# Kernel optimization log

Measured on AMD Instinct MI355X. Metric: run time of the kernel, lower is better.

Reference implementation:

```python
import jax, jax.numpy as jnp
import numpy as np

DIM = 192
HEADS = 8
B, H, W = 8, 128, 128

def _dwconv3x3(x, w):
    # x: [B,C,H,W], w: [C,1,3,3] depthwise
    return jax.lax.conv_general_dilated(
        x, w, window_strides=(1, 1), padding=((1, 1), (1, 1)),
        dimension_numbers=('NCHW', 'OIHW', 'NCHW'),
        feature_group_count=x.shape[1])

def _proj(x, pw, dw):
    # 1x1 pointwise (as einsum) followed by 3x3 depthwise
    y = jnp.einsum('bchw,oc->bohw', x, pw)
    return _dwconv3x3(y, dw)

def setup_inputs() -> dict:
    key = jax.random.key(0)
    ks = jax.random.split(key, 9)
    s_pw = 1.0 / np.sqrt(DIM)
    s_dw = 1.0 / 3.0
    return {
        'x_feat': jax.random.normal(ks[0], (B, DIM, H, W), jnp.float32),
        'y_feat': jax.random.normal(ks[1], (B, DIM, H, W), jnp.float32),
        'q_pw': jax.random.normal(ks[2], (DIM, DIM), jnp.float32) * s_pw,
        'q_dw': jax.random.normal(ks[3], (DIM, 1, 3, 3), jnp.float32) * s_dw,
        'k_pw': jax.random.normal(ks[4], (DIM, DIM), jnp.float32) * s_pw,
        'k_dw': jax.random.normal(ks[5], (DIM, 1, 3, 3), jnp.float32) * s_dw,
        'v_pw': jax.random.normal(ks[6], (DIM, DIM), jnp.float32) * s_pw,
        'v_dw': jax.random.normal(ks[7], (DIM, 1, 3, 3), jnp.float32) * s_dw,
        'proj_w': jax.random.normal(ks[8], (DIM, DIM), jnp.float32) * s_pw,
        'temperature': jnp.ones((HEADS, 1, 1), jnp.float32),
    }

def reference(x_feat, y_feat, q_pw, q_dw, k_pw, k_dw, v_pw, v_dw, proj_w, temperature):
    b, c, h, w = x_feat.shape
    ch = c // HEADS  # channels per head
    q = _proj(x_feat, q_pw, q_dw)
    k = _proj(y_feat, k_pw, k_dw)
    v = _proj(y_feat, v_pw, v_dw)
    # b (head c) h w -> b head c (h w)
    to_heads = lambda t: t.reshape(b, HEADS, ch, h * w)
    q, k, v = to_heads(q), to_heads(k), to_heads(v)
    # L2-normalize along token dim (torch F.normalize eps=1e-12)
    q = q / jnp.maximum(jnp.linalg.norm(q, axis=-1, keepdims=True), 1e-12)
    k = k / jnp.maximum(jnp.linalg.norm(k, axis=-1, keepdims=True), 1e-12)
    attn = jnp.einsum('bhcn,bhdn->bhcd', q, k) * temperature  # [b,heads,ch,ch]
    attn = jax.nn.softmax(attn, axis=-1)
    out = jnp.einsum('bhcd,bhdn->bhcn', attn, v)
    out = out.reshape(b, c, h, w)
    out = jnp.einsum('bchw,oc->bohw', out, proj_w)
    return out
```

## Files before the change

### kernel.cpp

```cpp
#include <hip/hip_runtime.h>
#include <hip/hip_bf16.h>

#define BATCH 8
#define CDIM 192
#define HEADS 8
#define CH 24
#define HH 128
#define WW 128
#define NPIX (HH*WW)
#define NELEM (BATCH*CDIM*NPIX)
#define NP4 (NPIX/4)

#define DSLAB 16
#define NJOBS 624

typedef __attribute__((ext_vector_type(8))) short bf16x8;
typedef __attribute__((ext_vector_type(4))) float f32x4;
typedef __attribute__((ext_vector_type(4))) unsigned int u32x4;
typedef __attribute__((ext_vector_type(8))) unsigned short u16x8;

#define UNIT 100663296ull
__device__ __align__(256) unsigned char g_pool[4 * UNIT + (16u << 20)];

#define OFF_T0   (0 * UNIT)
#define OFF_QB   (1 * UNIT)
#define OFF_KB   (2 * UNIT)
#define OFF_V    (3 * UNIT)
#define OFF_MISC (4 * UNIT)
#define OFF_PART (OFF_MISC)
#define OFF_S    (OFF_MISC + 2555904ull)
#define OFF_M    (OFF_S + 159744ull)
#define OFF_MF   (OFF_M + 1179648ull)

__device__ inline unsigned short bf_rne(float x) {
  unsigned u = __float_as_uint(x);
  unsigned r = (u + 0x7fffu + ((u >> 16) & 1u)) >> 16;
  return (unsigned short)r;
}
__device__ inline void f32_split(float x, unsigned short& h, unsigned short& l) {
  h = bf_rne(x);
  float hf = __uint_as_float(((unsigned)h) << 16);
  l = bf_rne(x - hf);
}

__global__ __launch_bounds__(64) void w_to_frag(const float* __restrict__ W,
                                                unsigned short* __restrict__ F,
                                                int nb) {
  const int b = blockIdx.x / 12, mf = blockIdx.x % 12;
  const int lane = threadIdx.x;
  const int row = mf * 16 + (lane & 15);
  const size_t lo = (size_t)nb * CDIM * CDIM;
#pragma unroll
  for (int ks = 0; ks < 6; ++ks) {
    const int k0 = ks * 32 + (lane >> 4) * 8;
    const float* src = W + ((size_t)b * CDIM + row) * CDIM + k0;
    bf16x8 hv, lv;
#pragma unroll
    for (int j = 0; j < 8; ++j) {
      unsigned short h, l;
      f32_split(src[j], h, l);
      hv[j] = (short)h;
      lv[j] = (short)l;
    }
    const size_t didx = (((size_t)(blockIdx.x) * 6 + ks) * 64 + lane) * 8;
    *(bf16x8*)(F + didx) = hv;
    *(bf16x8*)(F + lo + didx) = lv;
  }
}

__global__ __launch_bounds__(256, 2) void mfma_gemm192(
    const float* __restrict__ X,
    const unsigned short* __restrict__ WF, size_t w_lo,
    int w_bstride,
    float* __restrict__ Out) {
  const int bn = blockIdx.x;
  const int b = blockIdx.y;
  const int t = threadIdx.x;
  const int lane = t & 63, wid = t >> 6;
  const int wm = wid >> 1, wn = wid & 1;
  const int kq = lane >> 4;

  __shared__ float Xs[32][132];

  const size_t wbase = (size_t)b * w_bstride;
  const float* Xb = X + (size_t)b * CDIM * NPIX;
  const int col4 = (t & 31) * 4;
  const int r0 = t >> 5;
  const int pxl = wn * 64 + (lane & 15);

  f32x4 acc[6][4];
#pragma unroll
  for (int mi = 0; mi < 6; ++mi)
#pragma unroll
    for (int ni = 0; ni < 4; ++ni) acc[mi][ni] = (f32x4){0.f, 0.f, 0.f, 0.f};

  for (int ks = 0; ks < 6; ++ks) {
    float4 st[4];
#pragma unroll
    for (int p = 0; p < 4; ++p)
      st[p] = *(const float4*)(Xb + (size_t)(ks * 32 + r0 + 8 * p) * NPIX +
                               bn * 128 + col4);
#pragma unroll
    for (int p = 0; p < 4; ++p)
      *(float4*)&Xs[r0 + 8 * p][col4 ^ ((p & 1) << 4)] = st[p];
    __syncthreads();

    bf16x8 Ah[6], Al[6];
#pragma unroll
    for (int mi = 0; mi < 6; ++mi) {
      const int mf = wm * 6 + mi;
      const size_t idx = wbase + (((size_t)(mf * 6 + ks)) * 64 + lane) * 8;
      Ah[mi] = *(const bf16x8*)(WF + idx);
      Al[mi] = *(const bf16x8*)(WF + w_lo + idx);
    }

    u32x4 Bh[4], Bl[4];
#pragma unroll
    for (int ni = 0; ni < 4; ++ni) {
      const int pxs = (pxl + ni * 16) ^ ((kq & 1) << 4);
#pragma unroll
      for (int jp = 0; jp < 4; ++jp) {
        const float x0 = Xs[kq * 8 + 2 * jp][pxs];
        const float x1 = Xs[kq * 8 + 2 * jp + 1][pxs];
        const unsigned u0 = __float_as_uint(x0);
        const unsigned u1 = __float_as_uint(x1);
        Bh[ni][jp] = (u1 & 0xffff0000u) | (u0 >> 16);
        const float rr0 = x0 - __uint_as_float(u0 & 0xffff0000u);
        const float rr1 = x1 - __uint_as_float(u1 & 0xffff0000u);
        Bl[ni][jp] = ((unsigned)bf_rne(rr1) << 16) | (unsigned)bf_rne(rr0);
      }
    }
    __syncthreads();

#pragma unroll
    for (int mi = 0; mi < 6; ++mi)
#pragma unroll
      for (int ni = 0; ni < 4; ++ni) {
        const bf16x8 bh = __builtin_bit_cast(bf16x8, Bh[ni]);
        const bf16x8 bl = __builtin_bit_cast(bf16x8, Bl[ni]);
        acc[mi][ni] = __builtin_amdgcn_mfma_f32_16x16x32_bf16(
            Ah[mi], bh, acc[mi][ni], 0, 0, 0);
        acc[mi][ni] = __builtin_amdgcn_mfma_f32_16x16x32_bf16(
            Ah[mi], bl, acc[mi][ni], 0, 0, 0);
        acc[mi][ni] = __builtin_amdgcn_mfma_f32_16x16x32_bf16(
            Al[mi], bh, acc[mi][ni], 0, 0, 0);
      }
  }

  const int ocol = bn * 128 + wn * 64 + (lane & 15);
  const int orow = wm * 96 + (lane >> 4) * 4;
#pragma unroll
  for (int mi = 0; mi < 6; ++mi)
#pragma unroll
    for (int r = 0; r < 4; ++r) {
      const int och = orow + mi * 16 + r;
      float* dst = Out + ((size_t)b * CDIM + och) * NPIX + ocol;
#pragma unroll
      for (int ni = 0; ni < 4; ++ni) dst[ni * 16] = acc[mi][ni][r];
    }
}

__global__ __launch_bounds__(256) void dwconv(const float* __restrict__ In,
                                              const float* __restrict__ Wd,
                                              float* __restrict__ Out) {
  const int idx = blockIdx.x * 256 + threadIdx.x;
  const int x8 = (idx & 15) * 8;
  const int y = (idx >> 4) & 127;
  const int c = (idx >> 11) % CDIM;
  const int b = idx / (2048 * CDIM);

  const float* base = In + (size_t)(b * CDIM + c) * NPIX;
  float w[9];
#pragma unroll
  for (int i = 0; i < 9; ++i) w[i] = Wd[c * 9 + i];

  float a[8] = {0.f, 0.f, 0.f, 0.f, 0.f, 0.f, 0.f, 0.f};
#pragma unroll
  for (int dy = 0; dy < 3; ++dy) {
    const int yy = y + dy - 1;
    if (yy < 0 || yy > 127) continue;
    const float* row = base + yy * WW;
    const float lf = (x8 > 0) ? row[x8 - 1] : 0.f;
    const float4 m0 = *(const float4*)(row + x8);
    const float4 m1 = *(const float4*)(row + x8 + 4);
    const float rt = (x8 + 8 < WW) ? row[x8 + 8] : 0.f;
    const float w0 = w[dy * 3 + 0], w1 = w[dy * 3 + 1], w2 = w[dy * 3 + 2];
    a[0] += w0 * lf   + w1 * m0.x + w2 * m0.y;
    a[1] += w0 * m0.x + w1 * m0.y + w2 * m0.z;
    a[2] += w0 * m0.y + w1 * m0.z + w2 * m0.w;
    a[3] += w0 * m0.z + w1 * m0.w + w2 * m1.x;
    a[4] += w0 * m0.w + w1 * m1.x + w2 * m1.y;
    a[5] += w0 * m1.x + w1 * m1.y + w2 * m1.z;
    a[6] += w0 * m1.y + w1 * m1.z + w2 * m1.w;
    a[7] += w0 * m1.z + w1 * m1.w + w2 * rt;
  }
  float4 o0, o1;
  o0.x = a[0]; o0.y = a[1]; o0.z = a[2]; o0.w = a[3];
  o1.x = a[4]; o1.y = a[5]; o1.z = a[6]; o1.w = a[7];
  *(float4*)(Out + (size_t)idx * 8) = o0;
  *(float4*)(Out + (size_t)idx * 8 + 4) = o1;
}

__global__ __launch_bounds__(256) void dwconv_bf(const float* __restrict__ In,
                                                 const float* __restrict__ Wd,
                                                 unsigned short* __restrict__ Out) {
  const int idx = blockIdx.x * 256 + threadIdx.x;
  const int x8 = (idx & 15) * 8;
  const int y = (idx >> 4) & 127;
  const int c = (idx >> 11) % CDIM;
  const int b = idx / (2048 * CDIM);

  const float* base = In + (size_t)(b * CDIM + c) * NPIX;
  float w[9];
#pragma unroll
  for (int i = 0; i < 9; ++i) w[i] = Wd[c * 9 + i];

  float a[8] = {0.f, 0.f, 0.f, 0.f, 0.f, 0.f, 0.f, 0.f};
#pragma unroll
  for (int dy = 0; dy < 3; ++dy) {
    const int yy = y + dy - 1;
    if (yy < 0 || yy > 127) continue;
    const float* row = base + yy * WW;
    const float lf = (x8 > 0) ? row[x8 - 1] : 0.f;
    const float4 m0 = *(const float4*)(row + x8);
    const float4 m1 = *(const float4*)(row + x8 + 4);
    const float rt = (x8 + 8 < WW) ? row[x8 + 8] : 0.f;
    const float w0 = w[dy * 3 + 0], w1 = w[dy * 3 + 1], w2 = w[dy * 3 + 2];
    a[0] += w0 * lf   + w1 * m0.x + w2 * m0.y;
    a[1] += w0 * m0.x + w1 * m0.y + w2 * m0.z;
    a[2] += w0 * m0.y + w1 * m0.z + w2 * m0.w;
    a[3] += w0 * m0.z + w1 * m0.w + w2 * m1.x;
    a[4] += w0 * m0.w + w1 * m1.x + w2 * m1.y;
    a[5] += w0 * m1.x + w1 * m1.y + w2 * m1.z;
    a[6] += w0 * m1.y + w1 * m1.z + w2 * m1.w;
    a[7] += w0 * m1.z + w1 * m1.w + w2 * rt;
  }
  u16x8 hv, lv;
#pragma unroll
  for (int j = 0; j < 8; ++j) {
    unsigned short h, l;
    f32_split(a[j], h, l);
    hv[j] = h;
    lv[j] = l;
  }
  *(u16x8*)(Out + (size_t)idx * 8) = hv;
  *(u16x8*)(Out + NELEM + (size_t)idx * 8) = lv;
}

__global__ __launch_bounds__(256) void dots_mfma(
    const unsigned short* __restrict__ QF,
    const unsigned short* __restrict__ KF,
    float* __restrict__ Part) {
  const int bh = blockIdx.x;
  const int slab = blockIdx.y;
  const int b = bh >> 3, h = bh & 7;
  const int t = threadIdx.x;
  const int lane = t & 63, wid = t >> 6;

  const size_t rowbase = (size_t)(b * CDIM + h * CH);
  const int px0 = slab * 1024 + wid * 256;
  const int rr = lane & 15;
  const int j8 = (lane >> 4) * 8;

  f32x4 accx[2][2], aqq[2], aqhl[2], akk[2], akhl[2];
#pragma unroll
  for (int mi = 0; mi < 2; ++mi) {
#pragma unroll
    for (int ni = 0; ni < 2; ++ni) accx[mi][ni] = (f32x4){0.f, 0.f, 0.f, 0.f};
    aqq[mi] = (f32x4){0.f, 0.f, 0.f, 0.f};
    aqhl[mi] = (f32x4){0.f, 0.f, 0.f, 0.f};
    akk[mi] = (f32x4){0.f, 0.f, 0.f, 0.f};
    akhl[mi] = (f32x4){0.f, 0.f, 0.f, 0.f};
  }

  auto load_step = [&](int s, bf16x8 (&qh)[2], bf16x8 (&ql)[2],
                       bf16x8 (&kh)[2], bf16x8 (&kl)[2]) {
    const int px = px0 + s * 32 + j8;
#pragma unroll
    for (int mi = 0; mi < 2; ++mi) {
      const size_t off = (rowbase + mi * 16 + rr) * (size_t)NPIX + px;
      qh[mi] = *(const bf16x8*)(QF + off);
      ql[mi] = *(const bf16x8*)(QF + NELEM + off);
      kh[mi] = *(const bf16x8*)(KF + off);
      kl[mi] = *(const bf16x8*)(KF + NELEM + off);
    }
  };
  auto mfma_step = [&](bf16x8 (&qh)[2], bf16x8 (&ql)[2], bf16x8 (&kh)[2],
                       bf16x8 (&kl)[2]) {
#pragma unroll
    for (int mi = 0; mi < 2; ++mi) {
#pragma unroll
      for (int ni = 0; ni < 2; ++ni) {
        accx[mi][ni] = __builtin_amdgcn_mfma_f32_16x16x32_bf16(
            qh[mi], kh[ni], accx[mi][ni], 0, 0, 0);
        accx[mi][ni] = __builtin_amdgcn_mfma_f32_16x16x32_bf16(
            qh[mi], kl[ni], accx[mi][ni], 0, 0, 0);
        accx[mi][ni] = __builtin_amdgcn_mfma_f32_16x16x32_bf16(
            ql[mi], kh[ni], accx[mi][ni], 0, 0, 0);
      }
      aqq[mi] = __builtin_amdgcn_mfma_f32_16x16x32_bf16(qh[mi], qh[mi],
                                                        aqq[mi], 0, 0, 0);
      aqhl[mi] = __builtin_amdgcn_mfma_f32_16x16x32_bf16(qh[mi], ql[mi],
                                                         aqhl[mi], 0, 0, 0);
      akk[mi] = __builtin_amdgcn_mfma_f32_16x16x32_bf16(kh[mi], kh[mi],
                                                        akk[mi], 0, 0, 0);
      akhl[mi] = __builtin_amdgcn_mfma_f32_16x16x32_bf16(kh[mi], kl[mi],
                                                         akhl[mi], 0, 0, 0);
    }
  };

  bf16x8 Aqh[2], Aql[2], Akh[2], Akl[2];
  bf16x8 Bqh[2], Bql[2], Bkh[2], Bkl[2];
  load_step(0, Aqh, Aql, Akh, Akl);
#pragma unroll
  for (int s = 0; s < 8; s += 2) {
    if (s + 1 < 8) load_step(s + 1, Bqh, Bql, Bkh, Bkl);
    mfma_step(Aqh, Aql, Akh, Akl);
    if (s + 2 < 8) load_step(s + 2, Aqh, Aql, Akh, Akl);
    mfma_step(Bqh, Bql, Bkh, Bkl);
  }

  __shared__ float xls[4][24][24];
  __shared__ float qls[4][24], kls[4][24];
  const int col = lane & 15;
  const int rbase = (lane >> 4) * 4;
#pragma unroll
  for (int mi = 0; mi < 2; ++mi) {
#pragma unroll
    for (int ni = 0; ni < 2; ++ni) {
      const int d = ni * 16 + col;
      if (d < 24) {
#pragma unroll
        for (int r = 0; r < 4; ++r) {
          const int c = mi * 16 + rbase + r;
          if (c < 24) xls[wid][c][d] = accx[mi][ni][r];
        }
      }
    }
    const int cc = mi * 16 + col;
    const int rd = col - rbase;
    if (cc < 24 && rd >= 0 && rd < 4) {
      qls[wid][cc] = aqq[mi][rd] + 2.f * aqhl[mi][rd];
      kls[wid][cc] = akk[mi][rd] + 2.f * akhl[mi][rd];
    }
  }
  __syncthreads();

  float* P = Part + ((size_t)bh * DSLAB + slab) * NJOBS;
  for (int j = t; j < 576; j += 256) {
    const int c = j / 24, d = j % 24;
    P[j] = xls[0][c][d] + xls[1][c][d] + xls[2][c][d] + xls[3][c][d];
  }
  if (t < 24) P[576 + t] = qls[0][t] + qls[1][t] + qls[2][t] + qls[3][t];
  else if (t >= 32 && t < 56) {
    const int c = t - 32;
    P[600 + c] = kls[0][c] + kls[1][c] + kls[2][c] + kls[3][c];
  }
}

__global__ __launch_bounds__(640) void dots_reduce(const float* __restrict__ Part,
                                                   float* __restrict__ S) {
  const int bh = blockIdx.x;
  const int job = threadIdx.x;
  if (job >= NJOBS) return;
  float s = 0.f;
  for (int i = 0; i < DSLAB; ++i)
    s += Part[((size_t)bh * DSLAB + i) * NJOBS + job];
  S[bh * NJOBS + job] = s;
}

__global__ __launch_bounds__(576) void build_M(const float* __restrict__ S,
                                               const float* __restrict__ PW,
                                               const float* __restrict__ Temp,
                                               float* __restrict__ M) {
  const int b = blockIdx.x, h = blockIdx.y;
  const int bh = b * 8 + h;
  __shared__ float att[CH][CH];
  __shared__ float qn[CH], kn[CH];
  const int t = threadIdx.x;
  const float* Sb = S + (size_t)bh * NJOBS;

  if (t < CH) {
    qn[t] = fmaxf(sqrtf(Sb[576 + t]), 1e-12f);
    kn[t] = fmaxf(sqrtf(Sb[600 + t]), 1e-12f);
  }
  __syncthreads();
  const float temp = Temp[h];
  if (t < 576) {
    const int c = t / 24, d = t % 24;
    att[c][d] = Sb[t] / (qn[c] * kn[d]) * temp;
  }
  __syncthreads();
  if (t < CH) {
    float mx = -1e30f;
    for (int d = 0; d < CH; ++d) mx = fmaxf(mx, att[t][d]);
    float sum = 0.f;
    for (int d = 0; d < CH; ++d) {
      const float e = __expf(att[t][d] - mx);
      att[t][d] = e;
      sum += e;
    }
    const float inv = 1.f / sum;
    for (int d = 0; d < CH; ++d) att[t][d] *= inv;
  }
  __syncthreads();
  for (int i = t; i < CDIM * CH; i += 576) {
    const int o = i / CH, d = i % CH;
    float s = 0.f;
#pragma unroll
    for (int c = 0; c < CH; ++c) s += PW[o * CDIM + h * CH + c] * att[c][d];
    M[((size_t)b * CDIM + o) * CDIM + h * CH + d] = s;
  }
}


extern "C" void kernel_launch(void* const* d_in, const int* in_sizes, int n_in,
                              void* d_out, int out_size, void* d_ws, size_t ws_size,
                              hipStream_t stream) {
  const float* x_feat = (const float*)d_in[0];
  const float* y_feat = (const float*)d_in[1];
  const float* q_pw   = (const float*)d_in[2];
  const float* q_dw   = (const float*)d_in[3];
  const float* k_pw   = (const float*)d_in[4];
  const float* k_dw   = (const float*)d_in[5];
  const float* v_pw   = (const float*)d_in[6];
  const float* v_dw   = (const float*)d_in[7];
  const float* proj_w = (const float*)d_in[8];
  const float* temp   = (const float*)d_in[9];
  float* out = (float*)d_out;

  unsigned char* pool;
  (void)hipGetSymbolAddress((void**)&pool, HIP_SYMBOL(g_pool));
  float* t0 = (float*)(pool + OFF_T0);
  unsigned short* QB = (unsigned short*)(pool + OFF_QB);
  unsigned short* KB = (unsigned short*)(pool + OFF_KB);
  float* v  = (float*)(pool + OFF_V);
  float* part = (float*)(pool + OFF_PART);
  float* S    = (float*)(pool + OFF_S);
  float* M    = (float*)(pool + OFF_M);
  unsigned short* MF = (unsigned short*)(pool + OFF_MF);

  unsigned short* WQF = MF + 2ull * 8 * CDIM * CDIM;
  unsigned short* WKF = WQF + 2ull * CDIM * CDIM;
  unsigned short* WVF = WKF + 2ull * CDIM * CDIM;

  const size_t w1_lo = (size_t)1 * CDIM * CDIM;
  const size_t w8_lo = (size_t)8 * CDIM * CDIM;

  const dim3 ggrid(NPIX / 128, BATCH);
  const int dwgrid = (NELEM / 8) / 256;

  w_to_frag<<<12, 64, 0, stream>>>(q_pw, WQF, 1);
  w_to_frag<<<12, 64, 0, stream>>>(k_pw, WKF, 1);
  w_to_frag<<<12, 64, 0, stream>>>(v_pw, WVF, 1);

  mfma_gemm192<<<ggrid, 256, 0, stream>>>(x_feat, WQF, w1_lo, 0, t0);
  dwconv_bf<<<dwgrid, 256, 0, stream>>>(t0, q_dw, QB);
  mfma_gemm192<<<ggrid, 256, 0, stream>>>(y_feat, WKF, w1_lo, 0, t0);
  dwconv_bf<<<dwgrid, 256, 0, stream>>>(t0, k_dw, KB);

  dots_mfma<<<dim3(64, DSLAB), 256, 0, stream>>>(QB, KB, part);
  dots_reduce<<<64, 640, 0, stream>>>(part, S);
  build_M<<<dim3(BATCH, HEADS), 576, 0, stream>>>(S, proj_w, temp, M);
  w_to_frag<<<8 * 12, 64, 0, stream>>>(M, MF, 8);

  mfma_gemm192<<<ggrid, 256, 0, stream>>>(y_feat, WVF, w1_lo, 0, t0);
  dwconv<<<dwgrid, 256, 0, stream>>>(t0, v_dw, v);

  mfma_gemm192<<<ggrid, 256, 0, stream>>>(v, MF, w8_lo, CDIM * CDIM, out);
}
```

Baseline: 425.9 us.

## Drop LDS staging in pointwise GEMM and halve pixel tile to 64

New measurement: 501.5 us. +17.8%, slower.

```diff
diff --git a/kernel.cpp b/kernel.cpp
--- a/kernel.cpp
+++ b/kernel.cpp
@@ -80,48 +80,25 @@
   const int wm = wid >> 1, wn = wid & 1;
   const int kq = lane >> 4;
 
-  __shared__ float Xs[32][132];
-
   const size_t wbase = (size_t)b * w_bstride;
-  const float* Xb = X + (size_t)b * CDIM * NPIX;
-  const int col4 = (t & 31) * 4;
-  const int r0 = t >> 5;
-  const int pxl = wn * 64 + (lane & 15);
-
-  f32x4 acc[6][4];
+  const float* Xb = X + (size_t)b * CDIM * NPIX + bn * 64;
+  const int pxl = wn * 32 + (lane & 15);
+
+  f32x4 acc[6][2];
 #pragma unroll
   for (int mi = 0; mi < 6; ++mi)
 #pragma unroll
-    for (int ni = 0; ni < 4; ++ni) acc[mi][ni] = (f32x4){0.f, 0.f, 0.f, 0.f};
+    for (int ni = 0; ni < 2; ++ni) acc[mi][ni] = (f32x4){0.f, 0.f, 0.f, 0.f};
 
   for (int ks = 0; ks < 6; ++ks) {
-    float4 st[4];
-#pragma unroll
-    for (int p = 0; p < 4; ++p)
-      st[p] = *(const float4*)(Xb + (size_t)(ks * 32 + r0 + 8 * p) * NPIX +
-                               bn * 128 + col4);
-#pragma unroll
-    for (int p = 0; p < 4; ++p)
-      *(float4*)&Xs[r0 + 8 * p][col4 ^ ((p & 1) << 4)] = st[p];
-    __syncthreads();
-
-    bf16x8 Ah[6], Al[6];
-#pragma unroll
-    for (int mi = 0; mi < 6; ++mi) {
-      const int mf = wm * 6 + mi;
-      const size_t idx = wbase + (((size_t)(mf * 6 + ks)) * 64 + lane) * 8;
-      Ah[mi] = *(const bf16x8*)(WF + idx);
-      Al[mi] = *(const bf16x8*)(WF + w_lo + idx);
-    }
-
-    u32x4 Bh[4], Bl[4];
-#pragma unroll
-    for (int ni = 0; ni < 4; ++ni) {
-      const int pxs = (pxl + ni * 16) ^ ((kq & 1) << 4);
+    u32x4 Bh[2], Bl[2];
+#pragma unroll
+    for (int ni = 0; ni < 2; ++ni) {
+      const float* colp = Xb + (size_t)(ks * 32 + kq * 8) * NPIX + pxl + ni * 16;
 #pragma unroll
       for (int jp = 0; jp < 4; ++jp) {
-        const float x0 = Xs[kq * 8 + 2 * jp][pxs];
-        const float x1 = Xs[kq * 8 + 2 * jp + 1][pxs];
+        const float x0 = colp[(size_t)(2 * jp) * NPIX];
+        const float x1 = colp[(size_t)(2 * jp + 1) * NPIX];
         const unsigned u0 = __float_as_uint(x0);
         const unsigned u1 = __float_as_uint(x1);
         Bh[ni][jp] = (u1 & 0xffff0000u) | (u0 >> 16);
@@ -130,24 +107,27 @@
         Bl[ni][jp] = ((unsigned)bf_rne(rr1) << 16) | (unsigned)bf_rne(rr0);
       }
     }
-    __syncthreads();
-
-#pragma unroll
-    for (int mi = 0; mi < 6; ++mi)
-#pragma unroll
-      for (int ni = 0; ni < 4; ++ni) {
-        const bf16x8 bh = __builtin_bit_cast(bf16x8, Bh[ni]);
-        const bf16x8 bl = __builtin_bit_cast(bf16x8, Bl[ni]);
-        acc[mi][ni] = __builtin_amdgcn_mfma_f32_16x16x32_bf16(
-            Ah[mi], bh, acc[mi][ni], 0, 0, 0);
-        acc[mi][ni] = __builtin_amdgcn_mfma_f32_16x16x32_bf16(
-            Ah[mi], bl, acc[mi][ni], 0, 0, 0);
-        acc[mi][ni] = __builtin_amdgcn_mfma_f32_16x16x32_bf16(
-            Al[mi], bh, acc[mi][ni], 0, 0, 0);
-      }
-  }
-
-  const int ocol = bn * 128 + wn * 64 + (lane & 15);
+    const bf16x8 bh0 = __builtin_bit_cast(bf16x8, Bh[0]);
+    const bf16x8 bl0 = __builtin_bit_cast(bf16x8, Bl[0]);
+    const bf16x8 bh1 = __builtin_bit_cast(bf16x8, Bh[1]);
+    const bf16x8 bl1 = __builtin_bit_cast(bf16x8, Bl[1]);
+
+#pragma unroll
+    for (int mi = 0; mi < 6; ++mi) {
+      const int mf = wm * 6 + mi;
+      const size_t idx = wbase + (((size_t)(mf * 6 + ks)) * 64 + lane) * 8;
+      const bf16x8 Ah = *(const bf16x8*)(WF + idx);
+      const bf16x8 Al = *(const bf16x8*)(WF + w_lo + idx);
+      acc[mi][0] = __builtin_amdgcn_mfma_f32_16x16x32_bf16(Ah, bh0, acc[mi][0], 0, 0, 0);
+      acc[mi][0] = __builtin_amdgcn_mfma_f32_16x16x32_bf16(Ah, bl0, acc[mi][0], 0, 0, 0);
+      acc[mi][0] = __builtin_amdgcn_mfma_f32_16x16x32_bf16(Al, bh0, acc[mi][0], 0, 0, 0);
+      acc[mi][1] = __builtin_amdgcn_mfma_f32_16x16x32_bf16(Ah, bh1, acc[mi][1], 0, 0, 0);
+      acc[mi][1] = __builtin_amdgcn_mfma_f32_16x16x32_bf16(Ah, bl1, acc[mi][1], 0, 0, 0);
+      acc[mi][1] = __builtin_amdgcn_mfma_f32_16x16x32_bf16(Al, bh1, acc[mi][1], 0, 0, 0);
+    }
+  }
+
+  const int ocol = bn * 64 + wn * 32 + (lane & 15);
   const int orow = wm * 96 + (lane >> 4) * 4;
 #pragma unroll
   for (int mi = 0; mi < 6; ++mi)
@@ -155,8 +135,8 @@
     for (int r = 0; r < 4; ++r) {
       const int och = orow + mi * 16 + r;
       float* dst = Out + ((size_t)b * CDIM + och) * NPIX + ocol;
-#pragma unroll
-      for (int ni = 0; ni < 4; ++ni) dst[ni * 16] = acc[mi][ni][r];
+      dst[0] = acc[mi][0][r];
+      dst[16] = acc[mi][1][r];
     }
 }
 
@@ -447,7 +427,7 @@
   const size_t w1_lo = (size_t)1 * CDIM * CDIM;
   const size_t w8_lo = (size_t)8 * CDIM * CDIM;
 
-  const dim3 ggrid(NPIX / 128, BATCH);
+  const dim3 ggrid(NPIX / 64, BATCH);
   const int dwgrid = (NELEM / 8) / 256;
 
   w_to_frag<<<12, 64, 0, stream>>>(q_pw, WQF, 1);
```
